# Optimization experiments

Measured on AMD Instinct MI355X. Metric: run time of the kernel, lower is better.

Reference implementation:

```python
import jax, jax.numpy as jnp
import numpy as np

E = 2048      # embed_dim = qk_dim = v_dim = proj_dim
H = 16        # n_head
D = 128       # head_dim
ROT = 64      # rotary_dim (partial rotary: ROT < D)
PAD = 50257   # pad_token_id in select_at_last_token
EPS = 1e-5    # layer_norm_epsilon


def _sincos(T):
    # fixed_pos_embedding (GPT-J style): [T, ROT//2] each
    inv_freq = 1.0 / (10000.0 ** (jnp.arange(0, ROT, 2, dtype=jnp.float32) / ROT))
    ang = jnp.arange(T, dtype=jnp.float32)[:, None] * inv_freq[None, :]
    return jnp.sin(ang), jnp.cos(ang)


def _rope(x, sin, cos):
    # x: [B,T,H,ROT]; sin/cos: [T, ROT//2]; repeat_interleave(2) on last dim
    sin2 = jnp.repeat(sin, 2, axis=-1)[None, :, None, :]
    cos2 = jnp.repeat(cos, 2, axis=-1)[None, :, None, :]
    x1 = x[..., ::2]
    x2 = x[..., 1::2]
    rot = jnp.stack((-x2, x1), axis=-1).reshape(x.shape)  # rotate_every_two
    return x * cos2 + rot * sin2


def setup_inputs() -> dict:
    key = jax.random.key(0)
    ks = jax.random.split(key, 8)
    B, S = 8, 2048
    s = 0.02
    return {
        "hidden_states": jax.random.normal(ks[0], (B, S, E), jnp.float32),
        "input_ids_with_pads": jax.random.randint(ks[1], (B, S), 0, PAD),
        "ln_w": jnp.ones((E,), jnp.float32),
        "ln_b": jnp.zeros((E,), jnp.float32),
        "q_w": jax.random.normal(ks[2], (E, E), jnp.float32) * s,
        "q_b": jnp.zeros((E,), jnp.float32),
        "k_w": jax.random.normal(ks[3], (E, E), jnp.float32) * s,
        "k_b": jnp.zeros((E,), jnp.float32),
        "v_w": jax.random.normal(ks[4], (E, E), jnp.float32) * s,
        "v_b": jnp.zeros((E,), jnp.float32),
        "out_w": jax.random.normal(ks[5], (E, E), jnp.float32) * s,
        "out_b": jnp.zeros((E,), jnp.float32),
    }


def reference(hidden_states, input_ids_with_pads, ln_w, ln_b,
              q_w, q_b, k_w, k_b, v_w, v_b, out_w, out_b):
    B, S, _ = hidden_states.shape
    # LayerNorm
    mu = jnp.mean(hidden_states, axis=-1, keepdims=True)
    var = jnp.mean(jnp.square(hidden_states - mu), axis=-1, keepdims=True)
    hs = (hidden_states - mu) * jax.lax.rsqrt(var + EPS) * ln_w + ln_b
    # select_at_last_token: index of last non-pad token per row
    ix = jnp.argmax(jnp.cumsum((input_ids_with_pads != PAD).astype(jnp.int32), axis=1), axis=1)  # [B]
    h_last = jnp.take_along_axis(hs, ix[:, None, None], axis=1)  # [B,1,E]
    # projections (pool_to_vector: single query token)
    q = h_last @ q_w.T + q_b           # [B,1,E]
    k = hs @ k_w.T + k_b               # [B,S,E]
    v = hs @ v_w.T + v_b               # [B,S,E]
    # split heads; rotary layout keeps [B,T,H,D] for q,k
    q = q.reshape(B, 1, H, D)
    k = k.reshape(B, S, H, D)
    v = v.reshape(B, S, H, D).transpose(0, 2, 1, 3)  # [B,H,S,D]
    # partial rotary on first ROT dims (query at position 0, keys 0..S-1)
    sin, cos = _sincos(S)
    q = jnp.concatenate([_rope(q[..., :ROT], sin[:1], cos[:1]), q[..., ROT:]], axis=-1)
    k = jnp.concatenate([_rope(k[..., :ROT], sin, cos), k[..., ROT:]], axis=-1)
    q = q.transpose(0, 2, 1, 3)  # [B,H,1,D]
    k = k.transpose(0, 2, 1, 3)  # [B,H,S,D]
    # GPT-Neo _attn: no 1/sqrt(d) scaling; `bias` buffer is all-ones so the
    # causal mask is all-True and masked_bias is never applied.
    scores = jnp.einsum('bhqd,bhkd->bhqk', q, k)   # [B,H,1,S]
    attn = jax.nn.softmax(scores, axis=-1)
    out = jnp.einsum('bhqk,bhkd->bhqd', attn, v)   # [B,H,1,D]
    out = out.transpose(0, 2, 1, 3).reshape(B, 1, H * D)  # merge heads
    out = out @ out_w.T + out_b                    # out_proj
    return out[:, 0, :]                            # squeeze(-2): [B,E]
```

## Files before the change

kernel.cpp:

```cpp
#include <hip/hip_runtime.h>
#include <hip/hip_bf16.h>
#include <cstdint>
#include <cstddef>


using bf16x8 = __attribute__((ext_vector_type(8))) __bf16;
using f32x4  = __attribute__((ext_vector_type(4))) float;

__device__ __forceinline__ unsigned short f2bf(float f) {
  unsigned u = __float_as_uint(f);
  u += 0x7fffu + ((u >> 16) & 1u);
  return (unsigned short)(u >> 16);
}

__device__ __forceinline__ void gld16(const void* g, void* l) {
  __builtin_amdgcn_global_load_lds((__attribute__((address_space(1))) void*)g,
                                   (__attribute__((address_space(3))) void*)l,
                                   16, 0, 0);
}

__global__ __launch_bounds__(256) void prep_kernel(
    const float* __restrict__ hidden, const int* __restrict__ ids,
    const float* __restrict__ gw, const float* __restrict__ gb,
    const float* __restrict__ kw, unsigned short* __restrict__ hs,
    unsigned short* __restrict__ Wk, float2* __restrict__ tab,
    float* __restrict__ hl, float* __restrict__ Z) {
  const int blk = blockIdx.x, tid = threadIdx.x;
  const int wave = tid >> 6, lane = tid & 63;

  if (blk < 16384) {
    const size_t row = blk;
    const float* xr = hidden + row * 2048;
    float4 a = ((const float4*)xr)[tid];
    float4 b = ((const float4*)xr)[tid + 256];
    float s  = a.x + a.y + a.z + a.w + b.x + b.y + b.z + b.w;
    float ss = a.x*a.x + a.y*a.y + a.z*a.z + a.w*a.w +
               b.x*b.x + b.y*b.y + b.z*b.z + b.w*b.w;
    for (int m = 1; m < 64; m <<= 1) { s += __shfl_xor(s, m); ss += __shfl_xor(ss, m); }
    __shared__ float rs[4], rss[4];
    if (lane == 0) { rs[wave] = s; rss[wave] = ss; }
    __syncthreads();
    s  = rs[0] + rs[1] + rs[2] + rs[3];
    ss = rss[0] + rss[1] + rss[2] + rss[3];
    const float mu = s * (1.f / 2048.f);
    const float var = ss * (1.f / 2048.f) - mu * mu;
    const float r = rsqrtf(var + 1e-5f);
    const int i0 = tid * 4, i1 = 1024 + tid * 4;
    ushort4 p0 = {f2bf((a.x - mu) * r * gw[i0 + 0] + gb[i0 + 0]),
                  f2bf((a.y - mu) * r * gw[i0 + 1] + gb[i0 + 1]),
                  f2bf((a.z - mu) * r * gw[i0 + 2] + gb[i0 + 2]),
                  f2bf((a.w - mu) * r * gw[i0 + 3] + gb[i0 + 3])};
    ushort4 p1 = {f2bf((b.x - mu) * r * gw[i1 + 0] + gb[i1 + 0]),
                  f2bf((b.y - mu) * r * gw[i1 + 1] + gb[i1 + 1]),
                  f2bf((b.z - mu) * r * gw[i1 + 2] + gb[i1 + 2]),
                  f2bf((b.w - mu) * r * gw[i1 + 3] + gb[i1 + 3])};
    *(ushort4*)(hs + row * 2048 + i0) = p0;
    *(ushort4*)(hs + row * 2048 + i1) = p1;
  } else if (blk < 18432) {
    const size_t i4 = (size_t)(blk - 16384) * 256 + tid;
    const int r = (int)(i4 >> 9);
    const int col4 = (int)(i4 & 511);
    const size_t src4 = ((size_t)((r >> 6) * 128 + (r & 63))) * 512 + col4;
    float4 v = ((const float4*)kw)[src4];
    ushort4 o = {f2bf(v.x), f2bf(v.y), f2bf(v.z), f2bf(v.w)};
    ((ushort4*)Wk)[i4] = o;
  } else if (blk < 18688) {
    const int t = (blk - 18432) * 8 + (tid >> 5);
    const int i = tid & 31;
    const float inv = exp2f(-(float)i * (13.287712379549449f / 32.f));
    const float ang = (float)t * inv;
    tab[t * 32 + i] = make_float2(sinf(ang), cosf(ang));
  } else {
    const int b = blk - 18688;
    if (tid < 16) Z[b * 16 + tid] = 0.f;
    int best = -1;
    for (int t = tid; t < 2048; t += 256)
      if (ids[b * 2048 + t] != 50257) best = (t > best) ? t : best;
    for (int m = 1; m < 64; m <<= 1) {
      int o = __shfl_xor(best, m);
      best = (o > best) ? o : best;
    }
    __shared__ int rb[4];
    if (lane == 0) rb[wave] = best;
    __syncthreads();
    int ix = rb[0];
    for (int w = 1; w < 4; ++w) ix = (rb[w] > ix) ? rb[w] : ix;
    ix = (ix < 0) ? 0 : ix;
    const float* xr = hidden + ((size_t)b * 2048 + ix) * 2048;
    float4 a = ((const float4*)xr)[tid];
    float4 c = ((const float4*)xr)[tid + 256];
    float s  = a.x + a.y + a.z + a.w + c.x + c.y + c.z + c.w;
    float ss = a.x*a.x + a.y*a.y + a.z*a.z + a.w*a.w +
               c.x*c.x + c.y*c.y + c.z*c.z + c.w*c.w;
    for (int m = 1; m < 64; m <<= 1) { s += __shfl_xor(s, m); ss += __shfl_xor(ss, m); }
    __shared__ float rs2[4], rss2[4];
    if (lane == 0) { rs2[wave] = s; rss2[wave] = ss; }
    __syncthreads();
    s  = rs2[0] + rs2[1] + rs2[2] + rs2[3];
    ss = rss2[0] + rss2[1] + rss2[2] + rss2[3];
    const float mu = s * (1.f / 2048.f);
    const float var = ss * (1.f / 2048.f) - mu * mu;
    const float r = rsqrtf(var + 1e-5f);
    const int i0 = tid * 4, i1 = 1024 + tid * 4;
    float* yo = hl + (size_t)b * 2048;
    yo[i0 + 0] = (a.x - mu) * r * gw[i0 + 0] + gb[i0 + 0];
    yo[i0 + 1] = (a.y - mu) * r * gw[i0 + 1] + gb[i0 + 1];
    yo[i0 + 2] = (a.z - mu) * r * gw[i0 + 2] + gb[i0 + 2];
    yo[i0 + 3] = (a.w - mu) * r * gw[i0 + 3] + gb[i0 + 3];
    yo[i1 + 0] = (c.x - mu) * r * gw[i1 + 0] + gb[i1 + 0];
    yo[i1 + 1] = (c.y - mu) * r * gw[i1 + 1] + gb[i1 + 1];
    yo[i1 + 2] = (c.z - mu) * r * gw[i1 + 2] + gb[i1 + 2];
    yo[i1 + 3] = (c.w - mu) * r * gw[i1 + 3] + gb[i1 + 3];
  }
}

__global__ __launch_bounds__(256) void gemv8_kernel(const float* __restrict__ X,
                                                    const float* __restrict__ W,
                                                    const float* __restrict__ bias,
                                                    float* __restrict__ Y) {
  const int tid = threadIdx.x, lane = tid & 63, wave = tid >> 6;
  const int e = blockIdx.x * 4 + wave;
  const float* wr = W + (size_t)e * 2048;
  float p[8] = {0, 0, 0, 0, 0, 0, 0, 0};
#pragma unroll
  for (int it = 0; it < 8; ++it) {
    const int k = it * 256 + lane * 4;
    float4 wv = *(const float4*)(wr + k);
#pragma unroll
    for (int b = 0; b < 8; ++b) {
      float4 xv = *(const float4*)(X + b * 2048 + k);
      p[b] += wv.x * xv.x + wv.y * xv.y + wv.z * xv.z + wv.w * xv.w;
    }
  }
#pragma unroll
  for (int b = 0; b < 8; ++b)
    for (int m = 1; m < 64; m <<= 1) p[b] += __shfl_xor(p[b], m);
  if (lane == 0) {
    const float bb = bias[e];
#pragma unroll
    for (int b = 0; b < 8; ++b) Y[(size_t)b * 2048 + e] = p[b] + bb;
  }
}

__global__ __launch_bounds__(256) void fold_c_kernel(
    const float* __restrict__ qv, const float* __restrict__ kw,
    const float* __restrict__ kb, unsigned short* __restrict__ Cpad,
    float* __restrict__ qkb) {
  const int bh = blockIdx.x, b = bh >> 4, h = bh & 15;
  const int tid = threadIdx.x;
  const float* qh = qv + ((size_t)b * 16 + h) * 128 + 64;
  const int e0 = tid * 8;
  float acc[8] = {0, 0, 0, 0, 0, 0, 0, 0};
  for (int c = 0; c < 64; ++c) {
    const float qc = qh[c];
    const float* row = kw + ((size_t)(h * 128 + 64 + c)) * 2048 + e0;
    float4 v0 = *(const float4*)(row);
    float4 v1 = *(const float4*)(row + 4);
    acc[0] += qc * v0.x; acc[1] += qc * v0.y; acc[2] += qc * v0.z; acc[3] += qc * v0.w;
    acc[4] += qc * v1.x; acc[5] += qc * v1.y; acc[6] += qc * v1.z; acc[7] += qc * v1.w;
  }
  unsigned short* dst = Cpad + ((size_t)b * 128 + h) * 2048 + e0;
  ushort4 o0 = {f2bf(acc[0]), f2bf(acc[1]), f2bf(acc[2]), f2bf(acc[3])};
  ushort4 o1 = {f2bf(acc[4]), f2bf(acc[5]), f2bf(acc[6]), f2bf(acc[7])};
  *(ushort4*)(dst) = o0;
  *(ushort4*)(dst + 4) = o1;
  if (tid < 64) {
    float p = kb[h * 128 + 64 + tid] * qh[tid];
    for (int m = 1; m < 64; m <<= 1) p += __shfl_xor(p, m);
    if (tid == 0) qkb[bh] = p;
  }
}

__global__ __launch_bounds__(256) void gemm_plain_kernel(
    const unsigned short* __restrict__ A, const unsigned short* __restrict__ Cpad,
    const float* __restrict__ qkb, float* __restrict__ spS) {
  constexpr int K = 2048;
  __shared__ unsigned short As[128 * 32];
  __shared__ unsigned short Bs[128 * 32];
  const int tid = threadIdx.x;
  const int lane = tid & 63, wave = tid >> 6;
  const int wr = wave >> 1, wc = wave & 1;
  const int bm = blockIdx.x;
  const int b = bm >> 4;

  const unsigned short* Ap = A + ((size_t)(bm * 128 + (tid >> 2))) * K + (tid & 3) * 8;
  const unsigned short* Bp = Cpad + ((size_t)b * 128 + (tid >> 2)) * K + (tid & 3) * 8;
  unsigned short* lA0 = As + wave * 512;
  unsigned short* lA1 = As + 2048 + wave * 512;
  unsigned short* lB0 = Bs + wave * 512;
  unsigned short* lB1 = Bs + 2048 + wave * 512;

  f32x4 acc[4][4];
#pragma unroll
  for (int i = 0; i < 4; ++i)
#pragma unroll
    for (int j = 0; j < 4; ++j) acc[i][j] = (f32x4){0.f, 0.f, 0.f, 0.f};

  const unsigned short* aPtr[4];
  const unsigned short* bPtr[4];
#pragma unroll
  for (int mi = 0; mi < 4; ++mi)
    aPtr[mi] = As + (wr * 64 + mi * 16 + (lane & 15)) * 32 + (lane >> 4) * 8;
#pragma unroll
  for (int ni = 0; ni < 4; ++ni)
    bPtr[ni] = Bs + (wc * 64 + ni * 16 + (lane & 15)) * 32 + (lane >> 4) * 8;

  for (int kt = 0; kt < K / 32; ++kt) {
    const int ko = kt * 32;
    gld16(Ap + ko,          lA0);
    gld16(Ap + ko + 64 * K, lA1);
    gld16(Bp + ko,          lB0);
    gld16(Bp + ko + 64 * K, lB1);
    __syncthreads();
    bf16x8 af[4], bfr[4];
#pragma unroll
    for (int mi = 0; mi < 4; ++mi) af[mi] = *(const bf16x8*)aPtr[mi];
#pragma unroll
    for (int ni = 0; ni < 4; ++ni) bfr[ni] = *(const bf16x8*)bPtr[ni];
#pragma unroll
    for (int mi = 0; mi < 4; ++mi)
#pragma unroll
      for (int ni = 0; ni < 4; ++ni)
        acc[mi][ni] = __builtin_amdgcn_mfma_f32_16x16x32_bf16(af[mi], bfr[ni],
                                                              acc[mi][ni], 0, 0, 0);
    __syncthreads();
  }

  if (wc == 0) {
    const int rg = lane >> 4, l15 = lane & 15;
    const float qk = qkb[b * 16 + l15];
#pragma unroll
    for (int mi = 0; mi < 4; ++mi)
#pragma unroll
      for (int r = 0; r < 4; ++r) {
        const int row = wr * 64 + mi * 16 + rg * 4 + r;
        spS[((size_t)bm * 128 + row) * 16 + l15] = acc[mi][0][r] + qk;
      }
  }
}

__global__ __launch_bounds__(256) void gemm_kscore_rot_kernel(
    const unsigned short* __restrict__ A, const unsigned short* __restrict__ W,
    const float* __restrict__ kb, const float* __restrict__ qv,
    const float2* __restrict__ tab, const float* __restrict__ spS,
    float* __restrict__ sw_t, float* __restrict__ Z) {
  constexpr int K = 2048;
  __shared__ unsigned short As[128 * 32];
  __shared__ unsigned short Bs[128 * 32];
  const int tid = threadIdx.x;
  const int lane = tid & 63, wave = tid >> 6;
  const int wr = wave >> 1, wc = wave & 1;
  const int bm = blockIdx.x, bn = blockIdx.y;

  const unsigned short* Ap = A + ((size_t)(bm * 128 + (tid >> 2))) * K + (tid & 3) * 8;
  const unsigned short* Bp = W + ((size_t)(bn * 128 + (tid >> 2))) * K + (tid & 3) * 8;
  unsigned short* lA0 = As + wave * 512;
  unsigned short* lA1 = As + 2048 + wave * 512;
  unsigned short* lB0 = Bs + wave * 512;
  unsigned short* lB1 = Bs + 2048 + wave * 512;

  f32x4 acc[4][4];
#pragma unroll
  for (int i = 0; i < 4; ++i)
#pragma unroll
    for (int j = 0; j < 4; ++j) acc[i][j] = (f32x4){0.f, 0.f, 0.f, 0.f};

  const unsigned short* aPtr[4];
  const unsigned short* bPtr[4];
#pragma unroll
  for (int mi = 0; mi < 4; ++mi)
    aPtr[mi] = As + (wr * 64 + mi * 16 + (lane & 15)) * 32 + (lane >> 4) * 8;
#pragma unroll
  for (int ni = 0; ni < 4; ++ni)
    bPtr[ni] = Bs + (wc * 64 + ni * 16 + (lane & 15)) * 32 + (lane >> 4) * 8;

  for (int kt = 0; kt < K / 32; ++kt) {
    const int ko = kt * 32;
    gld16(Ap + ko,          lA0);
    gld16(Ap + ko + 64 * K, lA1);
    gld16(Bp + ko,          lB0);
    gld16(Bp + ko + 64 * K, lB1);
    __syncthreads();
    bf16x8 af[4], bfr[4];
#pragma unroll
    for (int mi = 0; mi < 4; ++mi) af[mi] = *(const bf16x8*)aPtr[mi];
#pragma unroll
    for (int ni = 0; ni < 4; ++ni) bfr[ni] = *(const bf16x8*)bPtr[ni];
#pragma unroll
    for (int mi = 0; mi < 4; ++mi)
#pragma unroll
      for (int ni = 0; ni < 4; ++ni)
        acc[mi][ni] = __builtin_amdgcn_mfma_f32_16x16x32_bf16(af[mi], bfr[ni],
                                                              acc[mi][ni], 0, 0, 0);
    __syncthreads();
  }

  const int b  = bm >> 4;
  const int h  = bn * 2 + wc;
  const int s0 = (bm & 15) * 128;
  const int rg = lane >> 4, l15 = lane & 15;
  const float* qb  = qv + ((size_t)b * 16 + h) * 128;
  const float* kbh = kb + h * 128;
  float rowsum[4][4];
#pragma unroll
  for (int mi = 0; mi < 4; ++mi)
#pragma unroll
    for (int r = 0; r < 4; ++r) rowsum[mi][r] = 0.f;

  const float sgn = (l15 & 1) ? -1.f : 1.f;
#pragma unroll
  for (int ni = 0; ni < 4; ++ni) {
    const int c = ni * 16 + l15;
    const float qd   = qb[c];
    const float qps  = sgn * qb[c ^ 1];
    const float bias = kbh[c];
    const int i = c >> 1;
#pragma unroll
    for (int mi = 0; mi < 4; ++mi)
#pragma unroll
      for (int r = 0; r < 4; ++r) {
        const int t = s0 + wr * 64 + mi * 16 + rg * 4 + r;
        const float2 sc = tab[t * 32 + i];
        rowsum[mi][r] += (acc[mi][ni][r] + bias) * (qd * sc.y + qps * sc.x);
      }
  }
#pragma unroll
  for (int mi = 0; mi < 4; ++mi)
#pragma unroll
    for (int r = 0; r < 4; ++r) {
      float v = rowsum[mi][r];
      v += __shfl_xor(v, 1);
      v += __shfl_xor(v, 2);
      v += __shfl_xor(v, 4);
      v += __shfl_xor(v, 8);
      rowsum[mi][r] = v;
    }
  float zpart = 0.f;
  if (l15 == 0) {
#pragma unroll
    for (int mi = 0; mi < 4; ++mi)
#pragma unroll
      for (int r = 0; r < 4; ++r) {
        const int row = wr * 64 + mi * 16 + rg * 4 + r;
        const float sc = rowsum[mi][r] +
                         spS[((size_t)bm * 128 + row) * 16 + h];
        const float w = __expf(sc - 40.f);
        sw_t[((size_t)b * 2048 + s0 + row) * 16 + h] = w;
        zpart += w;
      }
    zpart += __shfl_xor(zpart, 16);
    zpart += __shfl_xor(zpart, 32);
    if (lane == 0) atomicAdd(&Z[b * 16 + h], zpart);
  }
}

__global__ __launch_bounds__(256) void attn_wsum_kernel(
    const unsigned short* __restrict__ hs, const float* __restrict__ sw_t,
    float* __restrict__ part) {
  const int b = blockIdx.x, ech = blockIdx.y, tc = blockIdx.z;
  const int tid = threadIdx.x;
  const int e = ech * 512 + tid * 2;
  __shared__ float sw[128 * 16];
  {
    const float4* src = (const float4*)(sw_t + ((size_t)b * 2048 + tc * 128) * 16);
    float4* dst = (float4*)sw;
    dst[tid] = src[tid];
    dst[tid + 256] = src[tid + 256];
  }
  __syncthreads();
  float a0[16], a1[16];
#pragma unroll
  for (int h = 0; h < 16; ++h) { a0[h] = 0.f; a1[h] = 0.f; }
  const unsigned short* hp = hs + ((size_t)b * 2048 + tc * 128) * 2048 + e;
#pragma unroll 2
  for (int tt = 0; tt < 128; ++tt) {
    const unsigned hv = *(const unsigned*)(hp + (size_t)tt * 2048);
    const float h0 = __uint_as_float(hv << 16);
    const float h1 = __uint_as_float(hv & 0xffff0000u);
    const float4 w0 = *(const float4*)(sw + tt * 16 + 0);
    const float4 w1 = *(const float4*)(sw + tt * 16 + 4);
    const float4 w2 = *(const float4*)(sw + tt * 16 + 8);
    const float4 w3 = *(const float4*)(sw + tt * 16 + 12);
    const float wv[16] = {w0.x, w0.y, w0.z, w0.w, w1.x, w1.y, w1.z, w1.w,
                          w2.x, w2.y, w2.z, w2.w, w3.x, w3.y, w3.z, w3.w};
#pragma unroll
    for (int h = 0; h < 16; ++h) {
      a0[h] += wv[h] * h0;
      a1[h] += wv[h] * h1;
    }
  }
#pragma unroll
  for (int h = 0; h < 16; ++h) {
    float2 st = {a0[h], a1[h]};
    *(float2*)(part + (((size_t)tc * 8 + b) * 16 + h) * 2048 + e) = st;
  }
}

__global__ __launch_bounds__(256) void attn_comb_kernel(
    const float* __restrict__ part, const float* __restrict__ Z,
    float* __restrict__ wsumN) {
  const int bh = blockIdx.x, b = bh >> 4, h = bh & 15;
  const float zi = 1.f / Z[bh];
  for (int e = threadIdx.x; e < 2048; e += 256) {
    float s = 0.f;
#pragma unroll
    for (int tc = 0; tc < 16; ++tc)
      s += part[(((size_t)tc * 8 + b) * 16 + h) * 2048 + e];
    wsumN[(size_t)bh * 2048 + e] = s * zi;
  }
}

__global__ __launch_bounds__(256) void attn_vgemv_kernel(
    const float* __restrict__ vw, const float* __restrict__ vb,
    const float* __restrict__ wsumN, float* __restrict__ aout) {
  const int tid = threadIdx.x, lane = tid & 63, wave = tid >> 6;
  const int gw = blockIdx.x * 4 + wave;
  const int h = gw >> 7, d = gw & 127;
  const float* vr = vw + (size_t)gw * 2048;
  float p[8] = {0, 0, 0, 0, 0, 0, 0, 0};
#pragma unroll
  for (int it = 0; it < 8; ++it) {
    const int k = it * 256 + lane * 4;
    float4 wv = *(const float4*)(vr + k);
#pragma unroll
    for (int b = 0; b < 8; ++b) {
      float4 xv = *(const float4*)(wsumN + ((size_t)b * 16 + h) * 2048 + k);
      p[b] += wv.x * xv.x + wv.y * xv.y + wv.z * xv.z + wv.w * xv.w;
    }
  }
#pragma unroll
  for (int b = 0; b < 8; ++b)
    for (int m = 1; m < 64; m <<= 1) p[b] += __shfl_xor(p[b], m);
  if (lane == 0) {
    const float bb = vb[gw];
#pragma unroll
    for (int b = 0; b < 8; ++b)
      aout[((size_t)b * 16 + h) * 128 + d] = p[b] + bb;
  }
}

extern "C" void kernel_launch(void* const* d_in, const int* in_sizes, int n_in,
                              void* d_out, int out_size, void* d_ws, size_t ws_size,
                              hipStream_t stream) {
  (void)in_sizes; (void)n_in; (void)out_size; (void)ws_size;
  const float* hidden = (const float*)d_in[0];
  const int*   ids    = (const int*)d_in[1];
  const float* ln_w   = (const float*)d_in[2];
  const float* ln_b   = (const float*)d_in[3];
  const float* q_w    = (const float*)d_in[4];
  const float* q_b    = (const float*)d_in[5];
  const float* k_w    = (const float*)d_in[6];
  const float* k_b    = (const float*)d_in[7];
  const float* v_w    = (const float*)d_in[8];
  const float* v_b    = (const float*)d_in[9];
  const float* out_w  = (const float*)d_in[10];
  const float* out_b  = (const float*)d_in[11];
  float* out = (float*)d_out;

  char* ws = (char*)d_ws;
  unsigned short* hs  = (unsigned short*)ws; ws += (size_t)16384 * 2048 * 2;
  unsigned short* Wk  = (unsigned short*)ws; ws += (size_t)1024 * 2048 * 2;
  unsigned short* Cpad = (unsigned short*)ws; ws += (size_t)8 * 128 * 2048 * 2;
  float2* sctab = (float2*)ws; ws += (size_t)2048 * 32 * 8;
  float* qv     = (float*)ws; ws += (size_t)8 * 2048 * 4;
  float* hl     = (float*)ws; ws += (size_t)8 * 2048 * 4;
  float* aout   = (float*)ws; ws += (size_t)8 * 2048 * 4;
  float* sw_t   = (float*)ws; ws += (size_t)8 * 2048 * 16 * 4;
  float* spS    = (float*)ws; ws += (size_t)16384 * 16 * 4;
  float* qkb    = (float*)ws; ws += 128 * 4;
  float* Zb     = (float*)ws; ws += 128 * 4;
  float* part   = (float*)ws; ws += (size_t)16 * 8 * 16 * 2048 * 4;
  float* wsumN  = (float*)ws; ws += (size_t)128 * 2048 * 4;

  prep_kernel<<<18696, 256, 0, stream>>>(hidden, ids, ln_w, ln_b, k_w,
                                         hs, Wk, sctab, hl, Zb);
  gemv8_kernel<<<512, 256, 0, stream>>>(hl, q_w, q_b, qv);
  fold_c_kernel<<<128, 256, 0, stream>>>(qv, k_w, k_b, Cpad, qkb);
  gemm_plain_kernel<<<128, 256, 0, stream>>>(hs, Cpad, qkb, spS);
  gemm_kscore_rot_kernel<<<dim3(128, 8), 256, 0, stream>>>(hs, Wk, k_b, qv,
                                                           sctab, spS, sw_t, Zb);
  attn_wsum_kernel<<<dim3(8, 4, 16), 256, 0, stream>>>(hs, sw_t, part);
  attn_comb_kernel<<<128, 256, 0, stream>>>(part, Zb, wsumN);
  attn_vgemv_kernel<<<512, 256, 0, stream>>>(v_w, v_b, wsumN, aout);
  gemv8_kernel<<<512, 256, 0, stream>>>(aout, out_w, out_b, out);
}
```

Baseline: 469.3 us.

## Retile rotary K-score GEMM to 256x256 with double-buffered swizzled LDS

Rewrites the rotary K-score GEMM to use 512-thread workgroups computing 256x256 tiles with K-step 64. It double-buffers global-to-LDS loads with explicit vmcnt waits, XOR-swizzles the LDS layout to avoid bank conflicts, and remaps block IDs for better L2 locality. The goal is to raise MFMA utilization and overlap memory with compute, replacing the small 128x128 tiles that had a full barrier every 32-wide K step. In exchange it uses 128KB of LDS and more accumulator registers per thread, which limits occupancy, and only 256 workgroups are launched.

```diff
diff --git a/kernel.cpp b/kernel.cpp
--- a/kernel.cpp
+++ b/kernel.cpp
@@ -18,6 +18,11 @@
                                    (__attribute__((address_space(3))) void*)l,
                                    16, 0, 0);
 }
+
+#define FENCE() asm volatile("" ::: "memory")
+#define SBAR()  { FENCE(); __builtin_amdgcn_s_barrier(); FENCE(); }
+#define VM8()   asm volatile("s_waitcnt vmcnt(8)" ::: "memory")
+#define VM0()   asm volatile("s_waitcnt vmcnt(0)" ::: "memory")
 
 __global__ __launch_bounds__(256) void prep_kernel(
     const float* __restrict__ hidden, const int* __restrict__ ids,
@@ -239,93 +244,125 @@
   }
 }
 
-__global__ __launch_bounds__(256) void gemm_kscore_rot_kernel(
+__global__ __launch_bounds__(512, 2) void gemm_kscore_rot_kernel(
     const unsigned short* __restrict__ A, const unsigned short* __restrict__ W,
     const float* __restrict__ kb, const float* __restrict__ qv,
     const float2* __restrict__ tab, const float* __restrict__ spS,
     float* __restrict__ sw_t, float* __restrict__ Z) {
   constexpr int K = 2048;
-  __shared__ unsigned short As[128 * 32];
-  __shared__ unsigned short Bs[128 * 32];
+  constexpr int NT = K / 64;
+  __shared__ unsigned short Ls[4 * 16384];
+
   const int tid = threadIdx.x;
   const int lane = tid & 63, wave = tid >> 6;
-  const int wr = wave >> 1, wc = wave & 1;
-  const int bm = blockIdx.x, bn = blockIdx.y;
-
-  const unsigned short* Ap = A + ((size_t)(bm * 128 + (tid >> 2))) * K + (tid & 3) * 8;
-  const unsigned short* Bp = W + ((size_t)(bn * 128 + (tid >> 2))) * K + (tid & 3) * 8;
-  unsigned short* lA0 = As + wave * 512;
-  unsigned short* lA1 = As + 2048 + wave * 512;
-  unsigned short* lB0 = Bs + wave * 512;
-  unsigned short* lB1 = Bs + 2048 + wave * 512;
-
-  f32x4 acc[4][4];
-#pragma unroll
-  for (int i = 0; i < 4; ++i)
+  const int wr = wave >> 2, wc = wave & 3;
+  const int l15 = lane & 15, lk = lane >> 4, l7 = lane & 7;
+
+  const int orig = blockIdx.x;
+  const int wgid = (orig & 7) * 32 + (orig >> 3);
+  const int bm = wgid >> 2;
+  const int bn = wgid & 3;
+
+  const int srow = tid >> 3;
+  const int scb  = (tid & 7) ^ (srow & 7);
+  const unsigned short* Asrc = A + ((size_t)(bm * 256 + srow)) * K + scb * 8;
+  const unsigned short* Bsrc = W + ((size_t)(bn * 256 + srow)) * K + scb * 8;
+  const int wave512 = wave * 512;
+
+  f32x4 acc[8][4];
+#pragma unroll
+  for (int i = 0; i < 8; ++i)
 #pragma unroll
     for (int j = 0; j < 4; ++j) acc[i][j] = (f32x4){0.f, 0.f, 0.f, 0.f};
 
-  const unsigned short* aPtr[4];
-  const unsigned short* bPtr[4];
-#pragma unroll
-  for (int mi = 0; mi < 4; ++mi)
-    aPtr[mi] = As + (wr * 64 + mi * 16 + (lane & 15)) * 32 + (lane >> 4) * 8;
-#pragma unroll
-  for (int ni = 0; ni < 4; ++ni)
-    bPtr[ni] = Bs + (wc * 64 + ni * 16 + (lane & 15)) * 32 + (lane >> 4) * 8;
-
-  for (int kt = 0; kt < K / 32; ++kt) {
-    const int ko = kt * 32;
-    gld16(Ap + ko,          lA0);
-    gld16(Ap + ko + 64 * K, lA1);
-    gld16(Bp + ko,          lB0);
-    gld16(Bp + ko + 64 * K, lB1);
-    __syncthreads();
-    bf16x8 af[4], bfr[4];
-#pragma unroll
-    for (int mi = 0; mi < 4; ++mi) af[mi] = *(const bf16x8*)aPtr[mi];
-#pragma unroll
-    for (int ni = 0; ni < 4; ++ni) bfr[ni] = *(const bf16x8*)bPtr[ni];
-#pragma unroll
-    for (int mi = 0; mi < 4; ++mi)
-#pragma unroll
-      for (int ni = 0; ni < 4; ++ni)
-        acc[mi][ni] = __builtin_amdgcn_mfma_f32_16x16x32_bf16(af[mi], bfr[ni],
-                                                              acc[mi][ni], 0, 0, 0);
-    __syncthreads();
-  }
-
-  const int b  = bm >> 4;
-  const int h  = bn * 2 + wc;
-  const int s0 = (bm & 15) * 128;
-  const int rg = lane >> 4, l15 = lane & 15;
+  int rowA[8], rowB[4];
+#pragma unroll
+  for (int mi = 0; mi < 8; ++mi) rowA[mi] = (wr * 128 + mi * 16 + l15) * 64;
+#pragma unroll
+  for (int nj = 0; nj < 4; ++nj) rowB[nj] = (wc * 64 + nj * 16 + l15) * 64;
+
+#pragma unroll
+  for (int p = 0; p < 4; ++p) {
+    gld16(Asrc + (size_t)p * 64 * K, Ls + p * 4096 + wave512);
+    gld16(Bsrc + (size_t)p * 64 * K, Ls + 16384 + p * 4096 + wave512);
+  }
+#pragma unroll
+  for (int p = 0; p < 4; ++p) {
+    gld16(Asrc + (size_t)p * 64 * K + 64, Ls + 32768 + p * 4096 + wave512);
+    gld16(Bsrc + (size_t)p * 64 * K + 64, Ls + 49152 + p * 4096 + wave512);
+  }
+  VM8();
+  SBAR();
+
+  for (int t = 0; t < NT; ++t) {
+    const unsigned short* bufA = Ls + (t & 1) * 32768;
+    const unsigned short* bufB = bufA + 16384;
+#pragma unroll
+    for (int ks = 0; ks < 2; ++ks) {
+      const int offk = ((((ks << 2) | lk) ^ l7) << 3);
+      bf16x8 af[8], bfr[4];
+#pragma unroll
+      for (int mi = 0; mi < 8; ++mi)
+        af[mi] = *(const bf16x8*)(bufA + rowA[mi] + offk);
+#pragma unroll
+      for (int nj = 0; nj < 4; ++nj)
+        bfr[nj] = *(const bf16x8*)(bufB + rowB[nj] + offk);
+#pragma unroll
+      for (int mi = 0; mi < 8; ++mi)
+#pragma unroll
+        for (int nj = 0; nj < 4; ++nj)
+          acc[mi][nj] = __builtin_amdgcn_mfma_f32_16x16x32_bf16(
+              af[mi], bfr[nj], acc[mi][nj], 0, 0, 0);
+    }
+    if (t == NT - 1) break;
+    SBAR();
+    if (t + 2 < NT) {
+      const int k0 = (t + 2) * 64;
+      unsigned short* dA = Ls + (t & 1) * 32768 + wave512;
+      unsigned short* dB = dA + 16384;
+#pragma unroll
+      for (int p = 0; p < 4; ++p) {
+        gld16(Asrc + (size_t)p * 64 * K + k0, dA + p * 4096);
+        gld16(Bsrc + (size_t)p * 64 * K + k0, dB + p * 4096);
+      }
+      VM8();
+    } else {
+      VM0();
+    }
+    SBAR();
+  }
+
+  const int b  = bm >> 3;
+  const int h  = bn * 4 + wc;
+  const int rg = lk;
   const float* qb  = qv + ((size_t)b * 16 + h) * 128;
   const float* kbh = kb + h * 128;
-  float rowsum[4][4];
-#pragma unroll
-  for (int mi = 0; mi < 4; ++mi)
+  float rowsum[8][4];
+#pragma unroll
+  for (int mi = 0; mi < 8; ++mi)
 #pragma unroll
     for (int r = 0; r < 4; ++r) rowsum[mi][r] = 0.f;
 
+  const int s0g = bm * 256 + wr * 128;
   const float sgn = (l15 & 1) ? -1.f : 1.f;
 #pragma unroll
-  for (int ni = 0; ni < 4; ++ni) {
-    const int c = ni * 16 + l15;
+  for (int nj = 0; nj < 4; ++nj) {
+    const int c = nj * 16 + l15;
     const float qd   = qb[c];
     const float qps  = sgn * qb[c ^ 1];
     const float bias = kbh[c];
     const int i = c >> 1;
 #pragma unroll
-    for (int mi = 0; mi < 4; ++mi)
+    for (int mi = 0; mi < 8; ++mi)
 #pragma unroll
       for (int r = 0; r < 4; ++r) {
-        const int t = s0 + wr * 64 + mi * 16 + rg * 4 + r;
-        const float2 sc = tab[t * 32 + i];
-        rowsum[mi][r] += (acc[mi][ni][r] + bias) * (qd * sc.y + qps * sc.x);
+        const int t = s0g + mi * 16 + rg * 4 + r;
+        const float2 sc = tab[(t & 2047) * 32 + i];
+        rowsum[mi][r] += (acc[mi][nj][r] + bias) * (qd * sc.y + qps * sc.x);
       }
   }
 #pragma unroll
-  for (int mi = 0; mi < 4; ++mi)
+  for (int mi = 0; mi < 8; ++mi)
 #pragma unroll
     for (int r = 0; r < 4; ++r) {
       float v = rowsum[mi][r];
@@ -338,14 +375,13 @@
   float zpart = 0.f;
   if (l15 == 0) {
 #pragma unroll
-    for (int mi = 0; mi < 4; ++mi)
+    for (int mi = 0; mi < 8; ++mi)
 #pragma unroll
       for (int r = 0; r < 4; ++r) {
-        const int row = wr * 64 + mi * 16 + rg * 4 + r;
-        const float sc = rowsum[mi][r] +
-                         spS[((size_t)bm * 128 + row) * 16 + h];
+        const int gr = s0g + mi * 16 + rg * 4 + r;
+        const float sc = rowsum[mi][r] + spS[(size_t)gr * 16 + h];
         const float w = __expf(sc - 40.f);
-        sw_t[((size_t)b * 2048 + s0 + row) * 16 + h] = w;
+        sw_t[(size_t)gr * 16 + h] = w;
         zpart += w;
       }
     zpart += __shfl_xor(zpart, 16);
@@ -477,8 +513,8 @@
   gemv8_kernel<<<512, 256, 0, stream>>>(hl, q_w, q_b, qv);
   fold_c_kernel<<<128, 256, 0, stream>>>(qv, k_w, k_b, Cpad, qkb);
   gemm_plain_kernel<<<128, 256, 0, stream>>>(hs, Cpad, qkb, spS);
-  gemm_kscore_rot_kernel<<<dim3(128, 8), 256, 0, stream>>>(hs, Wk, k_b, qv,
-                                                           sctab, spS, sw_t, Zb);
+  gemm_kscore_rot_kernel<<<256, 512, 0, stream>>>(hs, Wk, k_b, qv,
+                                                  sctab, spS, sw_t, Zb);
   attn_wsum_kernel<<<dim3(8, 4, 16), 256, 0, stream>>>(hs, sw_t, part);
   attn_comb_kernel<<<128, 256, 0, stream>>>(part, Zb, wsumN);
   attn_vgemv_kernel<<<512, 256, 0, stream>>>(v_w, v_b, wsumN, aout);
```

After: 441.5 us. 1.06x faster.
